# Kernel optimization log

Measured on AMD Instinct MI355X. Metric: run time of the kernel, lower is better.

## Reference

```python
import jax, jax.numpy as jnp
import numpy as np

C = 128      # input_dim
HEADS = 1    # inner_dim == input_dim (required by W_o channel counts)
INNER = C * HEADS
H = W = 80
EPS = 1e-5


def conv1x1(x, w, b):
    # x: [1,Cin,H,W], w: [Cout,Cin], b: [Cout]
    return jnp.einsum('bchw,oc->bohw', x, w) + b[None, :, None, None]


def bn_train(x, gamma, beta):
    # train-mode BatchNorm2d: per-channel stats over (B,H,W)
    mean = jnp.mean(x, axis=(0, 2, 3), keepdims=True)
    var = jnp.var(x, axis=(0, 2, 3), keepdims=True)
    xn = (x - mean) * jax.lax.rsqrt(var + EPS)
    return gamma[None, :, None, None] * xn + beta[None, :, None, None]


def proj(x, w, b, g, bt):
    return jax.nn.relu(bn_train(conv1x1(x, w, b), g, bt))


def setup_inputs() -> dict:
    key = jax.random.key(0)
    ks = jax.random.split(key, 12)
    d = {
        'query': jax.random.normal(ks[0], (1, C, H, W), jnp.float32),
        'key': jax.random.normal(ks[1], (1, C, H, W), jnp.float32),
        'value': jax.random.normal(ks[2], (1, C, H, W), jnp.float32),
        'pos_embedding': jax.random.normal(ks[3], (1, H, W), jnp.float32),
    }
    def lin(k, co, ci):
        return jax.random.normal(k, (co, ci), jnp.float32) * 0.02
    for name, k in zip(['q', 'k', 'v'], ks[4:7]):
        d['w' + name] = lin(k, INNER, C)
        d['b' + name] = jnp.zeros((INNER,), jnp.float32)
        d['g' + name] = jnp.ones((INNER,), jnp.float32)
        d['beta' + name] = jnp.zeros((INNER,), jnp.float32)
    d['wo1'] = lin(ks[7], C, INNER)
    d['bo1'] = jnp.zeros((C,), jnp.float32)
    d['go'] = jnp.ones((C,), jnp.float32)
    d['betao'] = jnp.zeros((C,), jnp.float32)
    d['wo2'] = lin(ks[8], C, INNER)
    d['bo2'] = jnp.zeros((C,), jnp.float32)
    return d


def reference(query, key, value, pos_embedding,
              wq, bq, gq, betaq,
              wk, bk, gk, betak,
              wv, bv, gv, betav,
              wo1, bo1, go, betao, wo2, bo2):
    dim = query.shape[1]
    q = proj(query, wq, bq, gq, betaq)   # [1,INNER,H,W]
    k = proj(key, wk, bk, gk, betak)
    v = proj(value, wv, bv, gv, betav)
    N = q.shape[2] * q.shape[3]
    # heads=1: rearrange 'b (c h) x y -> b h (x y) c' == flatten+transpose
    q2 = q.reshape(INNER, N).T           # [N, INNER]
    k2 = k.reshape(INNER, N).T
    v2 = v.reshape(INNER, N).T
    # pos context: pos repeated across all channels -> q2 @ ctx^T is an outer product
    pos = pos_embedding.reshape(N)
    ctx = jnp.sum(q2, axis=-1, keepdims=True) * pos[None, :]   # [N, N]
    score = (q2 @ k2.T) / jnp.sqrt(jnp.float32(dim)) + ctx
    attn = jax.nn.softmax(score, axis=-1)
    out = attn @ v2                      # [N, INNER]
    # buggy original rearrange: x = N, y = 1 -> spatial [N, 1]
    out = out.T.reshape(1, INNER, N, 1)
    h = jax.nn.relu(bn_train(conv1x1(out, wo1, bo1), go, betao))
    return conv1x1(h, wo2, bo2)          # [1, C, N, 1]
```

## Files before the change

### kernel.cpp

```cpp
#include <hip/hip_runtime.h>

#define NPIX 6400

typedef float f4 __attribute__((ext_vector_type(4)));
typedef float f16v __attribute__((ext_vector_type(16)));
typedef short bf16x8 __attribute__((ext_vector_type(8)));
typedef unsigned int u4 __attribute__((ext_vector_type(4)));
typedef unsigned int u2 __attribute__((ext_vector_type(2)));
typedef _Float16 h8 __attribute__((ext_vector_type(8)));
typedef _Float16 h4 __attribute__((ext_vector_type(4)));
typedef unsigned short u16;
typedef unsigned int u32;

__device__ __forceinline__ u16 f2bf(float f){
  union { float f; u32 u; } v; v.f = f;
  u32 r = v.u + 0x7fffu + ((v.u >> 16) & 1u);
  return (u16)(r >> 16);
}
__device__ __forceinline__ float bf2f(u16 h){
  union { u32 u; float f; } v; v.u = (u32)h << 16; return v.f;
}
__device__ __forceinline__ float exp2_hw(float x){ return __builtin_amdgcn_exp2f(x); }

__global__ __launch_bounds__(512, 1) void k_proj(
    const float* __restrict__ xq, const float* __restrict__ xk, const float* __restrict__ xv,
    const float* __restrict__ wq, const float* __restrict__ bq,
    const float* __restrict__ wk, const float* __restrict__ bk,
    const float* __restrict__ wv, const float* __restrict__ bv,
    u16* __restrict__ Y, float* __restrict__ psum, float* __restrict__ psq)
{
  __shared__ __align__(16) float wT[64][132];
  __shared__ __align__(16) float xt[64][132];
  __shared__ __align__(16) float red[2][16][128];
  const int bid = blockIdx.x;
  const int proj = bid / 50, pt = bid % 50;
  const float* x = (proj == 0) ? xq : ((proj == 1) ? xk : xv);
  const float* w = (proj == 0) ? wq : ((proj == 1) ? wk : wv);
  const float* b = (proj == 0) ? bq : ((proj == 1) ? bk : bv);
  const int t = threadIdx.x;
  const int o0 = (t & 31) * 4, p0 = (t >> 5) * 8;
  float acc[4][8];
  #pragma unroll
  for (int i = 0; i < 4; ++i)
    #pragma unroll
    for (int j = 0; j < 8; ++j) acc[i][j] = 0.f;
  for (int cc = 0; cc < 2; ++cc){
    __syncthreads();
    for (int idx = t; idx < 2048; idx += 512){
      int o = idx >> 4, c4 = (idx & 15) * 4;
      f4 wv4 = *(const f4*)&w[o * 128 + cc * 64 + c4];
      wT[c4 + 0][o] = wv4[0]; wT[c4 + 1][o] = wv4[1];
      wT[c4 + 2][o] = wv4[2]; wT[c4 + 3][o] = wv4[3];
    }
    for (int idx = t; idx < 2048; idx += 512){
      int c = idx >> 5, p4 = (idx & 31) * 4;
      *(f4*)&xt[c][p4] = *(const f4*)&x[(cc * 64 + c) * NPIX + pt * 128 + p4];
    }
    __syncthreads();
    for (int c = 0; c < 64; ++c){
      f4 w4 = *(const f4*)&wT[c][o0];
      f4 x0 = *(const f4*)&xt[c][p0];
      f4 x1 = *(const f4*)&xt[c][p0 + 4];
      #pragma unroll
      for (int i = 0; i < 4; ++i){
        float wi = w4[i];
        #pragma unroll
        for (int j = 0; j < 4; ++j){ acc[i][j] += wi * x0[j]; acc[i][4 + j] += wi * x1[j]; }
      }
    }
  }
  f4 b4 = *(const f4*)&b[o0];
  #pragma unroll
  for (int i = 0; i < 4; ++i)
    #pragma unroll
    for (int j = 0; j < 8; ++j) acc[i][j] += b4[i];
  #pragma unroll
  for (int i = 0; i < 4; ++i){
    float s = 0.f, q = 0.f;
    #pragma unroll
    for (int j = 0; j < 8; ++j){ s += acc[i][j]; q += acc[i][j] * acc[i][j]; }
    red[0][t >> 5][o0 + i] = s;
    red[1][t >> 5][o0 + i] = q;
  }
  __syncthreads();
  if (t < 128){
    float s = 0.f, q = 0.f;
    #pragma unroll
    for (int g = 0; g < 16; ++g){ s += red[0][g][t]; q += red[1][g][t]; }
    psum[(proj * 50 + pt) * 128 + t] = s;
    psq [(proj * 50 + pt) * 128 + t] = q;
  }
  u16* Yb = Y + (size_t)proj * NPIX * 128;
  if (proj < 2){
    #pragma unroll
    for (int j = 0; j < 8; ++j){
      u2 v;
      v[0] = (u32)f2bf(acc[0][j]) | ((u32)f2bf(acc[1][j]) << 16);
      v[1] = (u32)f2bf(acc[2][j]) | ((u32)f2bf(acc[3][j]) << 16);
      *(u2*)&Yb[(size_t)(pt * 128 + p0 + j) * 128 + o0] = v;
    }
  } else {
    #pragma unroll
    for (int i = 0; i < 4; ++i){
      u4 v;
      #pragma unroll
      for (int jj = 0; jj < 4; ++jj)
        v[jj] = (u32)f2bf(acc[i][jj * 2]) | ((u32)f2bf(acc[i][jj * 2 + 1]) << 16);
      *(u4*)&Yb[(size_t)(o0 + i) * NPIX + pt * 128 + p0] = v;
    }
  }
}

__global__ __launch_bounds__(512, 1) void k_norm(
    const u16* __restrict__ Y, const float* __restrict__ psum, const float* __restrict__ psq,
    const float* __restrict__ gq, const float* __restrict__ beq,
    const float* __restrict__ gk, const float* __restrict__ bek,
    const float* __restrict__ gv, const float* __restrict__ bev,
    u16* __restrict__ q2, u16* __restrict__ k2, u16* __restrict__ v2t,
    float* __restrict__ rowsumq)
{
  __shared__ float sc[128], sh[128];
  const int bid = blockIdx.x, t = threadIdx.x;
  const int proj = bid / 50, pt = bid % 50;
  if (t < 128){
    float s = 0.f, q = 0.f;
    for (int i = 0; i < 50; ++i){
      s += psum[(proj * 50 + i) * 128 + t];
      q += psq [(proj * 50 + i) * 128 + t];
    }
    float mean = s * (1.f / NPIX);
    float var  = q * (1.f / NPIX) - mean * mean;
    const float* g  = (proj == 0) ? gq : ((proj == 1) ? gk : gv);
    const float* be = (proj == 0) ? beq : ((proj == 1) ? bek : bev);
    float scale = g[t] * rsqrtf(var + 1e-5f);
    sc[t] = scale; sh[t] = be[t] - mean * scale;
  }
  __syncthreads();
  const u16* Yb = Y + (size_t)proj * NPIX * 128;
  const float qs_l2 = 0.12751700f;
  if (proj < 2){
    int row = pt * 128 + (t >> 2), o0 = (t & 3) * 32;
    const float oscale = (proj == 0) ? qs_l2 : 1.f;
    float rs = 0.f;
    u32 pkd[16];
    #pragma unroll
    for (int u = 0; u < 4; ++u){
      bf16x8 y8 = *(const bf16x8*)&Yb[(size_t)row * 128 + o0 + u * 8];
      #pragma unroll
      for (int e = 0; e < 8; ++e){
        int o = o0 + u * 8 + e;
        float v = fmaxf(bf2f((u16)y8[e]) * sc[o] + sh[o], 0.f);
        rs += v;
        float ov = v * oscale;
        if ((e & 1) == 0) pkd[u * 4 + (e >> 1)] = (u32)f2bf(ov);
        else pkd[u * 4 + (e >> 1)] |= ((u32)f2bf(ov) << 16);
      }
    }
    u16* dst = (proj == 0) ? q2 : k2;
    u4* dp = (u4*)(dst + (size_t)row * 128 + o0);
    #pragma unroll
    for (int u = 0; u < 4; ++u){
      u4 v; v[0] = pkd[u*4]; v[1] = pkd[u*4+1]; v[2] = pkd[u*4+2]; v[3] = pkd[u*4+3];
      dp[u] = v;
    }
    if (proj == 0){
      rs += __shfl_xor(rs, 1);
      rs += __shfl_xor(rs, 2);
      if ((t & 3) == 0) rowsumq[row] = rs * 1.4426950408889634f;
    }
  } else {
    int o = t >> 2, pc = pt * 128 + (t & 3) * 32;
    float scale = sc[o], shift = sh[o];
    u32 pkd[16];
    #pragma unroll
    for (int u = 0; u < 4; ++u){
      bf16x8 y8 = *(const bf16x8*)&Yb[(size_t)o * NPIX + pc + u * 8];
      #pragma unroll
      for (int e = 0; e < 8; ++e){
        float v = fmaxf(bf2f((u16)y8[e]) * scale + shift, 0.f);
        if ((e & 1) == 0) pkd[u * 4 + (e >> 1)] = (u32)f2bf(v);
        else pkd[u * 4 + (e >> 1)] |= ((u32)f2bf(v) << 16);
      }
    }
    u4* dp = (u4*)(v2t + (size_t)o * NPIX + pc);
    #pragma unroll
    for (int u = 0; u < 4; ++u){
      u4 v; v[0] = pkd[u*4]; v[1] = pkd[u*4+1]; v[2] = pkd[u*4+2]; v[3] = pkd[u*4+3];
      dp[u] = v;
    }
  }
}

template<int NKT>
__global__ __launch_bounds__(512, 2) void k_flash(
    const u16* __restrict__ q2, const u16* __restrict__ k2, const u16* __restrict__ v2t,
    const float* __restrict__ rowsumq, const float* __restrict__ pos,
    _Float16* __restrict__ Opart, float* __restrict__ Mout, float* __restrict__ Lout,
    int js)
{
  __shared__ __align__(16) u16 Kt[2][64 * 128];
  __shared__ __align__(16) u16 Vt[2][128 * 64];
  __shared__ __align__(16) float posT[2][64];
  const int bid = blockIdx.x;
  const int qb = bid / js, jsi = bid % js;
  const int kt0 = jsi * NKT;
  const int tid = threadIdx.x;
  const int ln = tid & 63, wid = tid >> 6;
  const int lo = ln & 31, hi = ln >> 5;
  const int qrow = qb * 256 + wid * 32 + lo;

  const int kc_j = tid >> 4, kc_c8 = tid & 15;
  const int vc_d = tid >> 3, vc_c8 = tid & 7;
  bf16x8 kreg0, kreg1, vreg0, vreg1; float posr = 0.f;
  auto stage_load = [&](int j0){
    kreg0 = *(const bf16x8*)(k2 + (size_t)(j0 + kc_j) * 128 + kc_c8 * 8);
    kreg1 = *(const bf16x8*)(k2 + (size_t)(j0 + kc_j + 32) * 128 + kc_c8 * 8);
    vreg0 = *(const bf16x8*)(v2t + (size_t)vc_d * NPIX + j0 + vc_c8 * 8);
    vreg1 = *(const bf16x8*)(v2t + (size_t)(vc_d + 64) * NPIX + j0 + vc_c8 * 8);
    if (tid < 64) posr = pos[j0 + tid];
  };
  auto stage_write = [&](int b){
    char* kb = (char*)&Kt[b][0];
    char* vb = (char*)&Vt[b][0];
    *(bf16x8*)(kb + kc_j * 256 + ((kc_c8 * 16) ^ ((kc_j & 15) << 4))) = kreg0;
    *(bf16x8*)(kb + (kc_j + 32) * 256 + ((kc_c8 * 16) ^ (((kc_j + 32) & 15) << 4))) = kreg1;
    *(bf16x8*)(vb + vc_d * 128 + ((vc_c8 * 16) ^ ((vc_d & 7) << 4))) = vreg0;
    *(bf16x8*)(vb + (vc_d + 64) * 128 + ((vc_c8 * 16) ^ (((vc_d + 64) & 7) << 4))) = vreg1;
    if (tid < 64) posT[b][tid] = posr;
  };

  bf16x8 qf[8];
  const u16* qp = q2 + (size_t)qrow * 128 + hi * 8;
  #pragma unroll
  for (int kk = 0; kk < 8; ++kk) qf[kk] = *(const bf16x8*)(qp + kk * 16);
  const float rsq_l2 = rowsumq[qrow];
  f16v accO[4];
  #pragma unroll
  for (int c = 0; c < 4; ++c)
    #pragma unroll
    for (int r = 0; r < 16; ++r) accO[c][r] = 0.f;
  float m = -1e30f, l = 0.f;

  stage_load(kt0 * 64);
  stage_write(0);
  __syncthreads();
  int cur = 0;

  #pragma unroll 2
  for (int kt = 0; kt < NKT; ++kt){
    const bool more = (kt + 1 < NKT);
    if (more) stage_load((kt0 + kt + 1) * 64);

    f16v aS0a, aS0b, aS1a, aS1b;
    #pragma unroll
    for (int r = 0; r < 16; ++r){ aS0a[r] = 0.f; aS0b[r] = 0.f; aS1a[r] = 0.f; aS1b[r] = 0.f; }
    {
      const char* kb0 = (const char*)&Kt[cur][0] + lo * 256;
      const char* kb1 = (const char*)&Kt[cur][0] + (32 + lo) * 256;
      const int sw = (lo & 15) << 4;
      #pragma unroll
      for (int kk = 0; kk < 4; ++kk){
        int boA = (kk * 32 + hi * 16) ^ sw;
        int boB = ((kk + 4) * 32 + hi * 16) ^ sw;
        bf16x8 kf0a = *(const bf16x8*)(kb0 + boA);
        bf16x8 kf1a = *(const bf16x8*)(kb1 + boA);
        bf16x8 kf0b = *(const bf16x8*)(kb0 + boB);
        bf16x8 kf1b = *(const bf16x8*)(kb1 + boB);
        aS0a = __builtin_amdgcn_mfma_f32_32x32x16_bf16(kf0a, qf[kk], aS0a, 0, 0, 0);
        aS1a = __builtin_amdgcn_mfma_f32_32x32x16_bf16(kf1a, qf[kk], aS1a, 0, 0, 0);
        aS0b = __builtin_amdgcn_mfma_f32_32x32x16_bf16(kf0b, qf[kk + 4], aS0b, 0, 0, 0);
        aS1b = __builtin_amdgcn_mfma_f32_32x32x16_bf16(kf1b, qf[kk + 4], aS1b, 0, 0, 0);
      }
    }
    float pv[32];
    float mx = -1e30f;
    #pragma unroll
    for (int jsb = 0; jsb < 2; ++jsb){
      #pragma unroll
      for (int g = 0; g < 4; ++g){
        f4 p4 = *(const f4*)&posT[cur][jsb * 32 + g * 8 + hi * 4];
        #pragma unroll
        for (int e = 0; e < 4; ++e){
          float sraw = jsb ? (aS1a[g * 4 + e] + aS1b[g * 4 + e])
                           : (aS0a[g * 4 + e] + aS0b[g * 4 + e]);
          float sv = sraw + rsq_l2 * p4[e];
          pv[jsb * 16 + g * 4 + e] = sv;
          mx = fmaxf(mx, sv);
        }
      }
    }
    mx = fmaxf(mx, __shfl_xor(mx, 32));
    if (!__all(mx - m <= 11.5f)){
      float mnew = fmaxf(m, mx);
      float corr = exp2_hw(m - mnew);
      m = mnew;
      l *= corr;
      #pragma unroll
      for (int c = 0; c < 4; ++c)
        #pragma unroll
        for (int r = 0; r < 16; ++r) accO[c][r] *= corr;
    }
    float ls = 0.f;
    u32 pk[16];
    #pragma unroll
    for (int i = 0; i < 16; ++i){
      float e0 = exp2_hw(pv[2 * i]     - m);
      float e1 = exp2_hw(pv[2 * i + 1] - m);
      ls += e0 + e1;
      pk[i] = (u32)f2bf(e0) | ((u32)f2bf(e1) << 16);
    }
    ls += __shfl_xor(ls, 32);
    l += ls;

    if (more) stage_write(cur ^ 1);

    #pragma unroll
    for (int w = 0; w < 4; ++w){
      const int b0 = (w >> 1) * 8 + (w & 1) * 4;
      u32 s0 = __shfl_xor(pk[b0], 32);
      u32 s1 = __shfl_xor(pk[b0 + 1], 32);
      u32 s2 = __shfl_xor(pk[b0 + 2], 32);
      u32 s3 = __shfl_xor(pk[b0 + 3], 32);
      union { bf16x8 v; u32 u[4]; } pf;
      pf.u[0] = hi ? s2 : pk[b0];
      pf.u[1] = hi ? s3 : pk[b0 + 1];
      pf.u[2] = hi ? pk[b0 + 2] : s0;
      pf.u[3] = hi ? pk[b0 + 3] : s1;
      #pragma unroll
      for (int c = 0; c < 4; ++c){
        int d = c * 32 + lo;
        bf16x8 vf = *(const bf16x8*)((const char*)&Vt[cur][0] + d * 128 + ((w * 32 + hi * 16) ^ ((d & 7) << 4)));
        accO[c] = __builtin_amdgcn_mfma_f32_32x32x16_bf16(vf, pf.v, accO[c], 0, 0, 0);
      }
    }
    if (more) __syncthreads();
    cur ^= 1;
  }
  if (hi == 0){
    Mout[jsi * NPIX + qrow] = m;
    Lout[jsi * NPIX + qrow] = l;
  }
  const float linv = 1.f / l;
  _Float16* Ob = Opart + ((size_t)jsi * NPIX + qrow) * 128;
  #pragma unroll
  for (int c = 0; c < 4; ++c){
    #pragma unroll
    for (int g = 0; g < 4; ++g){
      h4 hv;
      #pragma unroll
      for (int e = 0; e < 4; ++e) hv[e] = (_Float16)(accO[c][g * 4 + e] * linv);
      *(h4*)&Ob[c * 32 + g * 8 + hi * 4] = hv;
    }
  }
}

template<int JS>
__global__ __launch_bounds__(256, 1) void k_out1(
    const _Float16* __restrict__ Opart, const float* __restrict__ Mbuf, const float* __restrict__ Lbuf,
    const float* __restrict__ wo1, const float* __restrict__ bo1,
    float* __restrict__ Z, float* __restrict__ p2s, float* __restrict__ p2q)
{
  __shared__ __align__(16) u16 wl[128 * 128];
  __shared__ __align__(16) u16 Ct[32 * 128];
  const int tid = threadIdx.x;
  {
    const int o = tid >> 1, h = tid & 1;
    const float* wp = wo1 + o * 128 + h * 64;
    char* dst = (char*)wl + o * 256;
    const int sw = (o & 15) << 4;
    #pragma unroll
    for (int u = 0; u < 8; ++u){
      f4 a = *(const f4*)(wp + u * 8);
      f4 b = *(const f4*)(wp + u * 8 + 4);
      union { bf16x8 v; u16 s[8]; } cc;
      #pragma unroll
      for (int e = 0; e < 4; ++e){ cc.s[e] = f2bf(a[e]); cc.s[4 + e] = f2bf(b[e]); }
      *(bf16x8*)(dst + ((h * 128 + u * 16) ^ sw)) = cc.v;
    }
  }
  {
    const int px = tid >> 3, c16 = (tid & 7) * 16;
    const int P = blockIdx.x * 32 + px;
    float coef[JS];
    float mmax = -1e30f;
    #pragma unroll
    for (int s = 0; s < JS; ++s){ coef[s] = Mbuf[s * NPIX + P]; mmax = fmaxf(mmax, coef[s]); }
    float den = 0.f;
    #pragma unroll
    for (int s = 0; s < JS; ++s){
      float w = exp2_hw(coef[s] - mmax) * Lbuf[s * NPIX + P];
      coef[s] = w; den += w;
    }
    float inv = 1.f / den;
    float a[16];
    #pragma unroll
    for (int e = 0; e < 16; ++e) a[e] = 0.f;
    #pragma unroll
    for (int s = 0; s < JS; ++s){
      float w = coef[s] * inv;
      const _Float16* op = Opart + ((size_t)s * NPIX + P) * 128 + c16;
      h8 h0 = *(const h8*)op;
      h8 h1 = *(const h8*)(op + 8);
      #pragma unroll
      for (int e = 0; e < 8; ++e){ a[e] += w * (float)h0[e]; a[8 + e] += w * (float)h1[e]; }
    }
    union { bf16x8 v; u16 s[8]; } c0, c1;
    #pragma unroll
    for (int e = 0; e < 8; ++e){ c0.s[e] = f2bf(a[e]); c1.s[e] = f2bf(a[8 + e]); }
    char* crow = (char*)Ct + px * 256;
    const int sw = (px & 15) << 4;
    *(bf16x8*)(crow + ((c16 * 2) ^ sw)) = c0.v;
    *(bf16x8*)(crow + ((c16 * 2 + 16) ^ sw)) = c1.v;
  }
  __syncthreads();
  const int ln = tid & 63, wid = tid >> 6, lo = ln & 31, hi = ln >> 5;
  const int p = blockIdx.x * 32 + lo;
  bf16x8 bfr[8];
  {
    const char* crow = (const char*)Ct + lo * 256;
    const int sw = (lo & 15) << 4;
    #pragma unroll
    for (int kk = 0; kk < 8; ++kk)
      bfr[kk] = *(const bf16x8*)(crow + ((kk * 32 + hi * 16) ^ sw));
  }
  f16v acc;
  #pragma unroll
  for (int r = 0; r < 16; ++r) acc[r] = 0.f;
  {
    const int o = wid * 32 + lo;
    const char* wrow = (const char*)wl + o * 256;
    const int sw = (o & 15) << 4;
    #pragma unroll
    for (int kk = 0; kk < 8; ++kk){
      bf16x8 wf = *(const bf16x8*)(wrow + ((kk * 32 + hi * 16) ^ sw));
      acc = __builtin_amdgcn_mfma_f32_32x32x16_bf16(wf, bfr[kk], acc, 0, 0, 0);
    }
  }
  #pragma unroll
  for (int g = 0; g < 4; ++g){
    const int o2 = wid * 32 + g * 8 + hi * 4;
    f4 b4 = *(const f4*)&bo1[o2];
    f4 zv;
    #pragma unroll
    for (int e = 0; e < 4; ++e) zv[e] = acc[g * 4 + e] + b4[e];
    *(f4*)&Z[(size_t)p * 128 + o2] = zv;
    #pragma unroll
    for (int e = 0; e < 4; ++e){
      float sv = zv[e], qv = zv[e] * zv[e];
      #pragma unroll
      for (int msk = 1; msk < 32; msk <<= 1){ sv += __shfl_xor(sv, msk); qv += __shfl_xor(qv, msk); }
      if (lo == 0){
        p2s[blockIdx.x * 128 + o2 + e] = sv;
        p2q[blockIdx.x * 128 + o2 + e] = qv;
      }
    }
  }
}

__global__ __launch_bounds__(256, 1) void k_out2(
    const float* __restrict__ Z, const float* __restrict__ p2s, const float* __restrict__ p2q,
    const float* __restrict__ go, const float* __restrict__ beo,
    const float* __restrict__ wo2, const float* __restrict__ bo2,
    float* __restrict__ out)
{
  __shared__ __align__(16) u16 wl[128 * 128];
  __shared__ __align__(16) u16 Ct[32 * 128];
  __shared__ float sc2[128], sh2[128];
  const int tid = threadIdx.x;
  if (tid < 128){
    float s = 0.f, q = 0.f;
    for (int i = 0; i < 200; ++i){ s += p2s[i * 128 + tid]; q += p2q[i * 128 + tid]; }
    float mean = s * (1.f / NPIX);
    float var  = q * (1.f / NPIX) - mean * mean;
    float scale = go[tid] * rsqrtf(var + 1e-5f);
    sc2[tid] = scale; sh2[tid] = beo[tid] - mean * scale;
  }
  {
    const int o = tid >> 1, h = tid & 1;
    const float* wp = wo2 + o * 128 + h * 64;
    char* dst = (char*)wl + o * 256;
    const int sw = (o & 15) << 4;
    #pragma unroll
    for (int u = 0; u < 8; ++u){
      f4 a = *(const f4*)(wp + u * 8);
      f4 b = *(const f4*)(wp + u * 8 + 4);
      union { bf16x8 v; u16 s[8]; } cc;
      #pragma unroll
      for (int e = 0; e < 4; ++e){ cc.s[e] = f2bf(a[e]); cc.s[4 + e] = f2bf(b[e]); }
      *(bf16x8*)(dst + ((h * 128 + u * 16) ^ sw)) = cc.v;
    }
  }
  __syncthreads();
  {
    const int px = tid >> 3, c16 = (tid & 7) * 16;
    const int P = blockIdx.x * 32 + px;
    union { bf16x8 v; u16 s[8]; } c0, c1;
    #pragma unroll
    for (int u = 0; u < 4; ++u){
      f4 z = *(const f4*)&Z[(size_t)P * 128 + c16 + u * 4];
      f4 s4 = *(const f4*)&sc2[c16 + u * 4];
      f4 h4v = *(const f4*)&sh2[c16 + u * 4];
      #pragma unroll
      for (int e = 0; e < 4; ++e){
        u16 hb = f2bf(fmaxf(z[e] * s4[e] + h4v[e], 0.f));
        if (u < 2) c0.s[u * 4 + e] = hb; else c1.s[(u - 2) * 4 + e] = hb;
      }
    }
    char* crow = (char*)Ct + px * 256;
    const int sw = (px & 15) << 4;
    *(bf16x8*)(crow + ((c16 * 2) ^ sw)) = c0.v;
    *(bf16x8*)(crow + ((c16 * 2 + 16) ^ sw)) = c1.v;
  }
  __syncthreads();
  const int ln = tid & 63, wid = tid >> 6, lo = ln & 31, hi = ln >> 5;
  const int p = blockIdx.x * 32 + lo;
  bf16x8 bfH[8];
  {
    const char* crow = (const char*)Ct + lo * 256;
    const int sw = (lo & 15) << 4;
    #pragma unroll
    for (int kk = 0; kk < 8; ++kk)
      bfH[kk] = *(const bf16x8*)(crow + ((kk * 32 + hi * 16) ^ sw));
  }
  f16v acc;
  #pragma unroll
  for (int r = 0; r < 16; ++r) acc[r] = 0.f;
  {
    const int o = wid * 32 + lo;
    const char* wrow = (const char*)wl + o * 256;
    const int sw = (o & 15) << 4;
    #pragma unroll
    for (int kk = 0; kk < 8; ++kk){
      bf16x8 wf = *(const bf16x8*)(wrow + ((kk * 32 + hi * 16) ^ sw));
      acc = __builtin_amdgcn_mfma_f32_32x32x16_bf16(wf, bfH[kk], acc, 0, 0, 0);
    }
  }
  #pragma unroll
  for (int g = 0; g < 4; ++g){
    const int o3 = wid * 32 + g * 8 + hi * 4;
    f4 b4 = *(const f4*)&bo2[o3];
    #pragma unroll
    for (int e = 0; e < 4; ++e)
      out[(size_t)(o3 + e) * NPIX + p] = acc[g * 4 + e] + b4[e];
  }
}

extern "C" void kernel_launch(void* const* d_in, const int* in_sizes, int n_in,
                              void* d_out, int out_size, void* d_ws, size_t ws_size,
                              hipStream_t stream)
{
  const float* query = (const float*)d_in[0];
  const float* key_  = (const float*)d_in[1];
  const float* value = (const float*)d_in[2];
  const float* pos   = (const float*)d_in[3];
  const float* wq = (const float*)d_in[4];  const float* bq = (const float*)d_in[5];
  const float* gq = (const float*)d_in[6];  const float* betaq = (const float*)d_in[7];
  const float* wk = (const float*)d_in[8];  const float* bk = (const float*)d_in[9];
  const float* gk = (const float*)d_in[10]; const float* betak = (const float*)d_in[11];
  const float* wv = (const float*)d_in[12]; const float* bv = (const float*)d_in[13];
  const float* gv = (const float*)d_in[14]; const float* betav = (const float*)d_in[15];
  const float* wo1 = (const float*)d_in[16]; const float* bo1 = (const float*)d_in[17];
  const float* go  = (const float*)d_in[18]; const float* betao = (const float*)d_in[19];
  const float* wo2 = (const float*)d_in[20]; const float* bo2 = (const float*)d_in[21];

  const size_t fixed = 8576000;
  auto need = [&](int j) -> size_t {
    size_t ml = (size_t)j * 51200;
    size_t op = (size_t)j * 1638400;
    size_t ov = op > 4915200 ? op : (size_t)4915200;
    return fixed + ml + ov;
  };
  int js = 5;
  if (ws_size >= need(10)) js = 10;

  char* W = (char*)d_ws;
  size_t off = 0;
  auto alloc = [&](size_t n){ char* p = W + off; off += n; return p; };
  u16*  q2      = (u16*)alloc(1638400);
  u16*  k2      = (u16*)alloc(1638400);
  u16*  v2t     = (u16*)alloc(1638400);
  float* rowsumq= (float*)alloc(25600);
  float* psum   = (float*)alloc(76800);
  float* psq    = (float*)alloc(76800);
  float* Z      = (float*)alloc(3276800);
  float* p2s    = (float*)alloc(102400);
  float* p2q    = (float*)alloc(102400);
  float* Mbuf   = (float*)alloc((size_t)js * 25600);
  float* Lbuf   = (float*)alloc((size_t)js * 25600);
  u16*  Y       = (u16*)(W + off);
  _Float16* Opart = (_Float16*)(W + off);

  k_proj <<<dim3(150), dim3(512), 0, stream>>>(query, key_, value, wq, bq, wk, bk, wv, bv, Y, psum, psq);
  k_norm <<<dim3(150), dim3(512), 0, stream>>>(Y, psum, psq, gq, betaq, gk, betak, gv, betav, q2, k2, v2t, rowsumq);
  if (js == 10){
    k_flash<10><<<dim3(25 * 10), dim3(512), 0, stream>>>(q2, k2, v2t, rowsumq, pos, Opart, Mbuf, Lbuf, 10);
    k_out1<10><<<dim3(200), dim3(256), 0, stream>>>(Opart, Mbuf, Lbuf, wo1, bo1, Z, p2s, p2q);
  } else {
    k_flash<20><<<dim3(25 * 5), dim3(512), 0, stream>>>(q2, k2, v2t, rowsumq, pos, Opart, Mbuf, Lbuf, 5);
    k_out1<5><<<dim3(200), dim3(256), 0, stream>>>(Opart, Mbuf, Lbuf, wo1, bo1, Z, p2s, p2q);
  }
  k_out2 <<<dim3(200), dim3(256), 0, stream>>>(Z, p2s, p2q, go, betao, wo2, bo2, (float*)d_out);
}
```

Measured before the change: 87.43 us.

## Fuse projection+BN and out1+out2 via cooperative grid sync, use packed bf16 cvt

Result: slower. 142.4 us (+62.8%).

```diff
diff --git a/kernel.cpp b/kernel.cpp
--- a/kernel.cpp
+++ b/kernel.cpp
@@ -1,4 +1,7 @@
 #include <hip/hip_runtime.h>
+#include <hip/hip_cooperative_groups.h>
+
+namespace cg = cooperative_groups;
 
 #define NPIX 6400
 
@@ -12,26 +15,31 @@
 typedef unsigned short u16;
 typedef unsigned int u32;
 
-__device__ __forceinline__ u16 f2bf(float f){
-  union { float f; u32 u; } v; v.f = f;
-  u32 r = v.u + 0x7fffu + ((v.u >> 16) & 1u);
-  return (u16)(r >> 16);
+__device__ __forceinline__ u32 pk_bf16(float lo, float hi){
+  u32 r;
+  asm("v_cvt_pk_bf16_f32 %0, %1, %2" : "=v"(r) : "v"(lo), "v"(hi));
+  return r;
 }
 __device__ __forceinline__ float bf2f(u16 h){
   union { u32 u; float f; } v; v.u = (u32)h << 16; return v.f;
 }
 __device__ __forceinline__ float exp2_hw(float x){ return __builtin_amdgcn_exp2f(x); }
 
-__global__ __launch_bounds__(512, 1) void k_proj(
+__global__ __launch_bounds__(512, 1) void k_projnorm(
     const float* __restrict__ xq, const float* __restrict__ xk, const float* __restrict__ xv,
     const float* __restrict__ wq, const float* __restrict__ bq,
     const float* __restrict__ wk, const float* __restrict__ bk,
     const float* __restrict__ wv, const float* __restrict__ bv,
-    u16* __restrict__ Y, float* __restrict__ psum, float* __restrict__ psq)
+    const float* __restrict__ gq, const float* __restrict__ beq,
+    const float* __restrict__ gk, const float* __restrict__ bek,
+    const float* __restrict__ gv, const float* __restrict__ bev,
+    u16* __restrict__ q2, u16* __restrict__ k2, u16* __restrict__ v2t,
+    float* __restrict__ rowsumq, float* __restrict__ psum, float* __restrict__ psq)
 {
   __shared__ __align__(16) float wT[64][132];
   __shared__ __align__(16) float xt[64][132];
   __shared__ __align__(16) float red[2][16][128];
+  __shared__ float sc[128], sh[128];
   const int bid = blockIdx.x;
   const int proj = bid / 50, pt = bid % 50;
   const float* x = (proj == 0) ? xq : ((proj == 1) ? xk : xv);
@@ -90,38 +98,9 @@
     psum[(proj * 50 + pt) * 128 + t] = s;
     psq [(proj * 50 + pt) * 128 + t] = q;
   }
-  u16* Yb = Y + (size_t)proj * NPIX * 128;
-  if (proj < 2){
-    #pragma unroll
-    for (int j = 0; j < 8; ++j){
-      u2 v;
-      v[0] = (u32)f2bf(acc[0][j]) | ((u32)f2bf(acc[1][j]) << 16);
-      v[1] = (u32)f2bf(acc[2][j]) | ((u32)f2bf(acc[3][j]) << 16);
-      *(u2*)&Yb[(size_t)(pt * 128 + p0 + j) * 128 + o0] = v;
-    }
-  } else {
-    #pragma unroll
-    for (int i = 0; i < 4; ++i){
-      u4 v;
-      #pragma unroll
-      for (int jj = 0; jj < 4; ++jj)
-        v[jj] = (u32)f2bf(acc[i][jj * 2]) | ((u32)f2bf(acc[i][jj * 2 + 1]) << 16);
-      *(u4*)&Yb[(size_t)(o0 + i) * NPIX + pt * 128 + p0] = v;
-    }
-  }
-}
-
-__global__ __launch_bounds__(512, 1) void k_norm(
-    const u16* __restrict__ Y, const float* __restrict__ psum, const float* __restrict__ psq,
-    const float* __restrict__ gq, const float* __restrict__ beq,
-    const float* __restrict__ gk, const float* __restrict__ bek,
-    const float* __restrict__ gv, const float* __restrict__ bev,
-    u16* __restrict__ q2, u16* __restrict__ k2, u16* __restrict__ v2t,
-    float* __restrict__ rowsumq)
-{
-  __shared__ float sc[128], sh[128];
-  const int bid = blockIdx.x, t = threadIdx.x;
-  const int proj = bid / 50, pt = bid % 50;
+
+  cg::this_grid().sync();
+
   if (t < 128){
     float s = 0.f, q = 0.f;
     for (int i = 0; i < 50; ++i){
@@ -136,57 +115,46 @@
     sc[t] = scale; sh[t] = be[t] - mean * scale;
   }
   __syncthreads();
-  const u16* Yb = Y + (size_t)proj * NPIX * 128;
+  f4 scv = *(const f4*)&sc[o0];
+  f4 shv = *(const f4*)&sh[o0];
+  float vv[4][8];
+  #pragma unroll
+  for (int i = 0; i < 4; ++i)
+    #pragma unroll
+    for (int j = 0; j < 8; ++j)
+      vv[i][j] = fmaxf(acc[i][j] * scv[i] + shv[i], 0.f);
   const float qs_l2 = 0.12751700f;
   if (proj < 2){
-    int row = pt * 128 + (t >> 2), o0 = (t & 3) * 32;
-    const float oscale = (proj == 0) ? qs_l2 : 1.f;
-    float rs = 0.f;
-    u32 pkd[16];
-    #pragma unroll
-    for (int u = 0; u < 4; ++u){
-      bf16x8 y8 = *(const bf16x8*)&Yb[(size_t)row * 128 + o0 + u * 8];
-      #pragma unroll
-      for (int e = 0; e < 8; ++e){
-        int o = o0 + u * 8 + e;
-        float v = fmaxf(bf2f((u16)y8[e]) * sc[o] + sh[o], 0.f);
-        rs += v;
-        float ov = v * oscale;
-        if ((e & 1) == 0) pkd[u * 4 + (e >> 1)] = (u32)f2bf(ov);
-        else pkd[u * 4 + (e >> 1)] |= ((u32)f2bf(ov) << 16);
-      }
-    }
+    const float os = (proj == 0) ? qs_l2 : 1.f;
     u16* dst = (proj == 0) ? q2 : k2;
-    u4* dp = (u4*)(dst + (size_t)row * 128 + o0);
-    #pragma unroll
-    for (int u = 0; u < 4; ++u){
-      u4 v; v[0] = pkd[u*4]; v[1] = pkd[u*4+1]; v[2] = pkd[u*4+2]; v[3] = pkd[u*4+3];
-      dp[u] = v;
+    #pragma unroll
+    for (int j = 0; j < 8; ++j){
+      u2 v;
+      v[0] = pk_bf16(vv[0][j] * os, vv[1][j] * os);
+      v[1] = pk_bf16(vv[2][j] * os, vv[3][j] * os);
+      *(u2*)&dst[(size_t)(pt * 128 + p0 + j) * 128 + o0] = v;
     }
     if (proj == 0){
-      rs += __shfl_xor(rs, 1);
-      rs += __shfl_xor(rs, 2);
-      if ((t & 3) == 0) rowsumq[row] = rs * 1.4426950408889634f;
+      float rs[8];
+      #pragma unroll
+      for (int j = 0; j < 8; ++j) rs[j] = vv[0][j] + vv[1][j] + vv[2][j] + vv[3][j];
+      #pragma unroll
+      for (int msk = 1; msk < 32; msk <<= 1)
+        #pragma unroll
+        for (int j = 0; j < 8; ++j) rs[j] += __shfl_xor(rs[j], msk);
+      if ((t & 31) == 0)
+        #pragma unroll
+        for (int j = 0; j < 8; ++j)
+          rowsumq[pt * 128 + p0 + j] = rs[j] * 1.4426950408889634f;
     }
   } else {
-    int o = t >> 2, pc = pt * 128 + (t & 3) * 32;
-    float scale = sc[o], shift = sh[o];
-    u32 pkd[16];
-    #pragma unroll
-    for (int u = 0; u < 4; ++u){
-      bf16x8 y8 = *(const bf16x8*)&Yb[(size_t)o * NPIX + pc + u * 8];
-      #pragma unroll
-      for (int e = 0; e < 8; ++e){
-        float v = fmaxf(bf2f((u16)y8[e]) * scale + shift, 0.f);
-        if ((e & 1) == 0) pkd[u * 4 + (e >> 1)] = (u32)f2bf(v);
-        else pkd[u * 4 + (e >> 1)] |= ((u32)f2bf(v) << 16);
-      }
-    }
-    u4* dp = (u4*)(v2t + (size_t)o * NPIX + pc);
-    #pragma unroll
-    for (int u = 0; u < 4; ++u){
-      u4 v; v[0] = pkd[u*4]; v[1] = pkd[u*4+1]; v[2] = pkd[u*4+2]; v[3] = pkd[u*4+3];
-      dp[u] = v;
+    #pragma unroll
+    for (int i = 0; i < 4; ++i){
+      u4 v;
+      #pragma unroll
+      for (int jj = 0; jj < 4; ++jj)
+        v[jj] = pk_bf16(vv[i][jj * 2], vv[i][jj * 2 + 1]);
+      *(u4*)&v2t[(size_t)(o0 + i) * NPIX + pt * 128 + p0] = v;
     }
   }
 }
@@ -307,7 +275,7 @@
       float e0 = exp2_hw(pv[2 * i]     - m);
       float e1 = exp2_hw(pv[2 * i + 1] - m);
       ls += e0 + e1;
-      pk[i] = (u32)f2bf(e0) | ((u32)f2bf(e1) << 16);
+      pk[i] = pk_bf16(e0, e1);
     }
     ls += __shfl_xor(ls, 32);
     l += ls;
@@ -355,13 +323,18 @@
 }
 
 template<int JS>
-__global__ __launch_bounds__(256, 1) void k_out1(
+__global__ __launch_bounds__(256, 1) void k_out12(
     const _Float16* __restrict__ Opart, const float* __restrict__ Mbuf, const float* __restrict__ Lbuf,
     const float* __restrict__ wo1, const float* __restrict__ bo1,
-    float* __restrict__ Z, float* __restrict__ p2s, float* __restrict__ p2q)
+    const float* __restrict__ go, const float* __restrict__ beo,
+    const float* __restrict__ wo2, const float* __restrict__ bo2,
+    float* __restrict__ p2s, float* __restrict__ p2q,
+    float* __restrict__ out)
 {
   __shared__ __align__(16) u16 wl[128 * 128];
   __shared__ __align__(16) u16 Ct[32 * 128];
+  __shared__ __align__(16) float Zt[32][132];
+  __shared__ float sc2[128], sh2[128];
   const int tid = threadIdx.x;
   {
     const int o = tid >> 1, h = tid & 1;
@@ -372,9 +345,9 @@
     for (int u = 0; u < 8; ++u){
       f4 a = *(const f4*)(wp + u * 8);
       f4 b = *(const f4*)(wp + u * 8 + 4);
-      union { bf16x8 v; u16 s[8]; } cc;
-      #pragma unroll
-      for (int e = 0; e < 4; ++e){ cc.s[e] = f2bf(a[e]); cc.s[4 + e] = f2bf(b[e]); }
+      union { bf16x8 v; u32 uu[4]; } cc;
+      cc.uu[0] = pk_bf16(a[0], a[1]); cc.uu[1] = pk_bf16(a[2], a[3]);
+      cc.uu[2] = pk_bf16(b[0], b[1]); cc.uu[3] = pk_bf16(b[2], b[3]);
       *(bf16x8*)(dst + ((h * 128 + u * 16) ^ sw)) = cc.v;
     }
   }
@@ -404,9 +377,9 @@
       #pragma unroll
       for (int e = 0; e < 8; ++e){ a[e] += w * (float)h0[e]; a[8 + e] += w * (float)h1[e]; }
     }
-    union { bf16x8 v; u16 s[8]; } c0, c1;
-    #pragma unroll
-    for (int e = 0; e < 8; ++e){ c0.s[e] = f2bf(a[e]); c1.s[e] = f2bf(a[8 + e]); }
+    union { bf16x8 v; u32 uu[4]; } c0, c1;
+    #pragma unroll
+    for (int e = 0; e < 4; ++e){ c0.uu[e] = pk_bf16(a[e * 2], a[e * 2 + 1]); c1.uu[e] = pk_bf16(a[8 + e * 2], a[9 + e * 2]); }
     char* crow = (char*)Ct + px * 256;
     const int sw = (px & 15) << 4;
     *(bf16x8*)(crow + ((c16 * 2) ^ sw)) = c0.v;
@@ -414,59 +387,47 @@
   }
   __syncthreads();
   const int ln = tid & 63, wid = tid >> 6, lo = ln & 31, hi = ln >> 5;
-  const int p = blockIdx.x * 32 + lo;
-  bf16x8 bfr[8];
-  {
+  {
+    bf16x8 bfr[8];
     const char* crow = (const char*)Ct + lo * 256;
-    const int sw = (lo & 15) << 4;
+    const int swc = (lo & 15) << 4;
     #pragma unroll
     for (int kk = 0; kk < 8; ++kk)
-      bfr[kk] = *(const bf16x8*)(crow + ((kk * 32 + hi * 16) ^ sw));
-  }
-  f16v acc;
-  #pragma unroll
-  for (int r = 0; r < 16; ++r) acc[r] = 0.f;
-  {
+      bfr[kk] = *(const bf16x8*)(crow + ((kk * 32 + hi * 16) ^ swc));
+    f16v acc;
+    #pragma unroll
+    for (int r = 0; r < 16; ++r) acc[r] = 0.f;
     const int o = wid * 32 + lo;
     const char* wrow = (const char*)wl + o * 256;
-    const int sw = (o & 15) << 4;
+    const int sww = (o & 15) << 4;
     #pragma unroll
     for (int kk = 0; kk < 8; ++kk){
-      bf16x8 wf = *(const bf16x8*)(wrow + ((kk * 32 + hi * 16) ^ sw));
+      bf16x8 wf = *(const bf16x8*)(wrow + ((kk * 32 + hi * 16) ^ sww));
       acc = __builtin_amdgcn_mfma_f32_32x32x16_bf16(wf, bfr[kk], acc, 0, 0, 0);
     }
-  }
-  #pragma unroll
-  for (int g = 0; g < 4; ++g){
-    const int o2 = wid * 32 + g * 8 + hi * 4;
-    f4 b4 = *(const f4*)&bo1[o2];
-    f4 zv;
-    #pragma unroll
-    for (int e = 0; e < 4; ++e) zv[e] = acc[g * 4 + e] + b4[e];
-    *(f4*)&Z[(size_t)p * 128 + o2] = zv;
-    #pragma unroll
-    for (int e = 0; e < 4; ++e){
-      float sv = zv[e], qv = zv[e] * zv[e];
-      #pragma unroll
-      for (int msk = 1; msk < 32; msk <<= 1){ sv += __shfl_xor(sv, msk); qv += __shfl_xor(qv, msk); }
-      if (lo == 0){
-        p2s[blockIdx.x * 128 + o2 + e] = sv;
-        p2q[blockIdx.x * 128 + o2 + e] = qv;
+    #pragma unroll
+    for (int g = 0; g < 4; ++g){
+      const int o2 = wid * 32 + g * 8 + hi * 4;
+      f4 b4 = *(const f4*)&bo1[o2];
+      f4 zv;
+      #pragma unroll
+      for (int e = 0; e < 4; ++e) zv[e] = acc[g * 4 + e] + b4[e];
+      *(f4*)&Zt[lo][o2] = zv;
+      #pragma unroll
+      for (int e = 0; e < 4; ++e){
+        float sv = zv[e], qv = zv[e] * zv[e];
+        #pragma unroll
+        for (int msk = 1; msk < 32; msk <<= 1){ sv += __shfl_xor(sv, msk); qv += __shfl_xor(qv, msk); }
+        if (lo == 0){
+          p2s[blockIdx.x * 128 + o2 + e] = sv;
+          p2q[blockIdx.x * 128 + o2 + e] = qv;
+        }
       }
     }
   }
-}
-
-__global__ __launch_bounds__(256, 1) void k_out2(
-    const float* __restrict__ Z, const float* __restrict__ p2s, const float* __restrict__ p2q,
-    const float* __restrict__ go, const float* __restrict__ beo,
-    const float* __restrict__ wo2, const float* __restrict__ bo2,
-    float* __restrict__ out)
-{
-  __shared__ __align__(16) u16 wl[128 * 128];
-  __shared__ __align__(16) u16 Ct[32 * 128];
-  __shared__ float sc2[128], sh2[128];
-  const int tid = threadIdx.x;
+
+  cg::this_grid().sync();
+
   if (tid < 128){
     float s = 0.f, q = 0.f;
     for (int i = 0; i < 200; ++i){ s += p2s[i * 128 + tid]; q += p2q[i * 128 + tid]; }
@@ -484,27 +445,28 @@
     for (int u = 0; u < 8; ++u){
       f4 a = *(const f4*)(wp + u * 8);
       f4 b = *(const f4*)(wp + u * 8 + 4);
-      union { bf16x8 v; u16 s[8]; } cc;
-      #pragma unroll
-      for (int e = 0; e < 4; ++e){ cc.s[e] = f2bf(a[e]); cc.s[4 + e] = f2bf(b[e]); }
+      union { bf16x8 v; u32 uu[4]; } cc;
+      cc.uu[0] = pk_bf16(a[0], a[1]); cc.uu[1] = pk_bf16(a[2], a[3]);
+      cc.uu[2] = pk_bf16(b[0], b[1]); cc.uu[3] = pk_bf16(b[2], b[3]);
       *(bf16x8*)(dst + ((h * 128 + u * 16) ^ sw)) = cc.v;
     }
   }
   __syncthreads();
   {
     const int px = tid >> 3, c16 = (tid & 7) * 16;
-    const int P = blockIdx.x * 32 + px;
-    union { bf16x8 v; u16 s[8]; } c0, c1;
+    union { bf16x8 v; u32 uu[4]; } c0, c1;
     #pragma unroll
     for (int u = 0; u < 4; ++u){
-      f4 z = *(const f4*)&Z[(size_t)P * 128 + c16 + u * 4];
+      f4 z = *(const f4*)&Zt[px][c16 + u * 4];
       f4 s4 = *(const f4*)&sc2[c16 + u * 4];
       f4 h4v = *(const f4*)&sh2[c16 + u * 4];
-      #pragma unroll
-      for (int e = 0; e < 4; ++e){
-        u16 hb = f2bf(fmaxf(z[e] * s4[e] + h4v[e], 0.f));
-        if (u < 2) c0.s[u * 4 + e] = hb; else c1.s[(u - 2) * 4 + e] = hb;
-      }
+      float h0 = fmaxf(z[0] * s4[0] + h4v[0], 0.f);
+      float h1 = fmaxf(z[1] * s4[1] + h4v[1], 0.f);
+      float h2 = fmaxf(z[2] * s4[2] + h4v[2], 0.f);
+      float h3 = fmaxf(z[3] * s4[3] + h4v[3], 0.f);
+      u32 lo32 = pk_bf16(h0, h1), hi32 = pk_bf16(h2, h3);
+      if (u < 2){ c0.uu[u * 2] = lo32; c0.uu[u * 2 + 1] = hi32; }
+      else { c1.uu[(u - 2) * 2] = lo32; c1.uu[(u - 2) * 2 + 1] = hi32; }
     }
     char* crow = (char*)Ct + px * 256;
     const int sw = (px & 15) << 4;
@@ -512,36 +474,33 @@
     *(bf16x8*)(crow + ((c16 * 2 + 16) ^ sw)) = c1.v;
   }
   __syncthreads();
-  const int ln = tid & 63, wid = tid >> 6, lo = ln & 31, hi = ln >> 5;
-  const int p = blockIdx.x * 32 + lo;
-  bf16x8 bfH[8];
-  {
+  {
+    const int p = blockIdx.x * 32 + lo;
+    bf16x8 bfH[8];
     const char* crow = (const char*)Ct + lo * 256;
-    const int sw = (lo & 15) << 4;
+    const int swc = (lo & 15) << 4;
     #pragma unroll
     for (int kk = 0; kk < 8; ++kk)
-      bfH[kk] = *(const bf16x8*)(crow + ((kk * 32 + hi * 16) ^ sw));
-  }
-  f16v acc;
-  #pragma unroll
-  for (int r = 0; r < 16; ++r) acc[r] = 0.f;
-  {
+      bfH[kk] = *(const bf16x8*)(crow + ((kk * 32 + hi * 16) ^ swc));
+    f16v acc;
+    #pragma unroll
+    for (int r = 0; r < 16; ++r) acc[r] = 0.f;
     const int o = wid * 32 + lo;
     const char* wrow = (const char*)wl + o * 256;
-    const int sw = (o & 15) << 4;
+    const int sww = (o & 15) << 4;
     #pragma unroll
     for (int kk = 0; kk < 8; ++kk){
-      bf16x8 wf = *(const bf16x8*)(wrow + ((kk * 32 + hi * 16) ^ sw));
+      bf16x8 wf = *(const bf16x8*)(wrow + ((kk * 32 + hi * 16) ^ sww));
       acc = __builtin_amdgcn_mfma_f32_32x32x16_bf16(wf, bfH[kk], acc, 0, 0, 0);
     }
-  }
-  #pragma unroll
-  for (int g = 0; g < 4; ++g){
-    const int o3 = wid * 32 + g * 8 + hi * 4;
-    f4 b4 = *(const f4*)&bo2[o3];
-    #pragma unroll
-    for (int e = 0; e < 4; ++e)
-      out[(size_t)(o3 + e) * NPIX + p] = acc[g * 4 + e] + b4[e];
+    #pragma unroll
+    for (int g = 0; g < 4; ++g){
+      const int o3 = wid * 32 + g * 8 + hi * 4;
+      f4 b4 = *(const f4*)&bo2[o3];
+      #pragma unroll
+      for (int e = 0; e < 4; ++e)
+        out[(size_t)(o3 + e) * NPIX + p] = acc[g * 4 + e] + b4[e];
+    }
   }
 }
 
@@ -563,12 +522,9 @@
   const float* go  = (const float*)d_in[18]; const float* betao = (const float*)d_in[19];
   const float* wo2 = (const float*)d_in[20]; const float* bo2 = (const float*)d_in[21];
 
-  const size_t fixed = 8576000;
+  const size_t fixed = 5299200;
   auto need = [&](int j) -> size_t {
-    size_t ml = (size_t)j * 51200;
-    size_t op = (size_t)j * 1638400;
-    size_t ov = op > 4915200 ? op : (size_t)4915200;
-    return fixed + ml + ov;
+    return fixed + (size_t)j * 51200 + (size_t)j * 1638400;
   };
   int js = 5;
   if (ws_size >= need(10)) js = 10;
@@ -582,22 +538,37 @@
   float* rowsumq= (float*)alloc(25600);
   float* psum   = (float*)alloc(76800);
   float* psq    = (float*)alloc(76800);
-  float* Z      = (float*)alloc(3276800);
   float* p2s    = (float*)alloc(102400);
   float* p2q    = (float*)alloc(102400);
   float* Mbuf   = (float*)alloc((size_t)js * 25600);
   float* Lbuf   = (float*)alloc((size_t)js * 25600);
-  u16*  Y       = (u16*)(W + off);
-  _Float16* Opart = (_Float16*)(W + off);
-
-  k_proj <<<dim3(150), dim3(512), 0, stream>>>(query, key_, value, wq, bq, wk, bk, wv, bv, Y, psum, psq);
-  k_norm <<<dim3(150), dim3(512), 0, stream>>>(Y, psum, psq, gq, betaq, gk, betak, gv, betav, q2, k2, v2t, rowsumq);
+  _Float16* Opart = (_Float16*)alloc((size_t)js * 1638400);
+  float* outp   = (float*)d_out;
+
+  {
+    void* args[] = {
+      (void*)&query, (void*)&key_, (void*)&value,
+      (void*)&wq, (void*)&bq, (void*)&wk, (void*)&bk, (void*)&wv, (void*)&bv,
+      (void*)&gq, (void*)&betaq, (void*)&gk, (void*)&betak, (void*)&gv, (void*)&betav,
+      (void*)&q2, (void*)&k2, (void*)&v2t, (void*)&rowsumq, (void*)&psum, (void*)&psq
+    };
+    hipLaunchCooperativeKernel((void*)k_projnorm, dim3(150), dim3(512), args, 0, stream);
+  }
   if (js == 10){
-    k_flash<10><<<dim3(25 * 10), dim3(512), 0, stream>>>(q2, k2, v2t, rowsumq, pos, Opart, Mbuf, Lbuf, 10);
-    k_out1<10><<<dim3(200), dim3(256), 0, stream>>>(Opart, Mbuf, Lbuf, wo1, bo1, Z, p2s, p2q);
+    k_flash<10><<<dim3(250), dim3(512), 0, stream>>>(q2, k2, v2t, rowsumq, pos, Opart, Mbuf, Lbuf, 10);
+    void* args[] = {
+      (void*)&Opart, (void*)&Mbuf, (void*)&Lbuf, (void*)&wo1, (void*)&bo1,
+      (void*)&go, (void*)&betao, (void*)&wo2, (void*)&bo2,
+      (void*)&p2s, (void*)&p2q, (void*)&outp
+    };
+    hipLaunchCooperativeKernel((void*)(&k_out12<10>), dim3(200), dim3(256), args, 0, stream);
   } else {
-    k_flash<20><<<dim3(25 * 5), dim3(512), 0, stream>>>(q2, k2, v2t, rowsumq, pos, Opart, Mbuf, Lbuf, 5);
-    k_out1<5><<<dim3(200), dim3(256), 0, stream>>>(Opart, Mbuf, Lbuf, wo1, bo1, Z, p2s, p2q);
-  }
-  k_out2 <<<dim3(200), dim3(256), 0, stream>>>(Z, p2s, p2q, go, betao, wo2, bo2, (float*)d_out);
+    k_flash<20><<<dim3(125), dim3(512), 0, stream>>>(q2, k2, v2t, rowsumq, pos, Opart, Mbuf, Lbuf, 5);
+    void* args[] = {
+      (void*)&Opart, (void*)&Mbuf, (void*)&Lbuf, (void*)&wo1, (void*)&bo1,
+      (void*)&go, (void*)&betao, (void*)&wo2, (void*)&bo2,
+      (void*)&p2s, (void*)&p2q, (void*)&outp
+    };
+    hipLaunchCooperativeKernel((void*)(&k_out12<5>), dim3(200), dim3(256), args, 0, stream);
+  }
 }
```
